# Kernel tuning notes

Measured on AMD Instinct MI355X. Metric: run time of the kernel, lower is better.

The kernel has to match this reference:

```python
import jax, jax.numpy as jnp
import numpy as np

SEM_DIM = 256
AC_DIM = 36
CODEBOOK_SIZE = 8192
FSQ_LEVELS = 21
COMMIT_COST = 0.25
HALF = (FSQ_LEVELS - 1) / 2.0  # 10.0
EPS = 0.001


def setup_inputs() -> dict:
    key = jax.random.key(0)
    k1, k2 = jax.random.split(key)
    z = jax.random.normal(k1, (8, SEM_DIM + AC_DIM, 4096), dtype=jnp.float32)
    lim = 1.0 / CODEBOOK_SIZE
    codebook = jax.random.uniform(k2, (CODEBOOK_SIZE, SEM_DIM), dtype=jnp.float32,
                                  minval=-lim, maxval=lim)
    return {"z": z, "codebook": codebook}


def _round_ste(x):
    return x + jax.lax.stop_gradient(jnp.round(x) - x)


def _vq(z_sem, codebook):
    # z_sem: (B, D, T), codebook: (K, D)
    B, D, T = z_sem.shape
    z_flat = jnp.transpose(z_sem, (0, 2, 1)).reshape(B * T, D)  # (N, D)
    # pairwise squared distances via matmul: ||z||^2 - 2 z.W^T + ||W||^2
    dists = (jnp.sum(z_flat * z_flat, axis=1, keepdims=True)
             - 2.0 * jnp.matmul(z_flat, codebook.T)
             + jnp.sum(codebook * codebook, axis=1)[None, :])  # (N, K)
    indices = jnp.argmin(dists, axis=1)  # (N,)
    z_q_flat = codebook[indices]  # (N, D) gather
    z_q = jnp.transpose(z_q_flat.reshape(B, T, D), (0, 2, 1))  # (B, D, T)
    codebook_loss = jnp.mean((z_q - jax.lax.stop_gradient(z_sem)) ** 2)
    commitment_loss = COMMIT_COST * jnp.mean((jax.lax.stop_gradient(z_q) - z_sem) ** 2)
    loss = codebook_loss + commitment_loss
    z_q_ste = z_sem + jax.lax.stop_gradient(z_q - z_sem)  # straight-through
    return z_q_ste, indices.reshape(B, T), loss


def _fsq(z_ac):
    z_b = jnp.tanh(z_ac) * (HALF + EPS)
    z_q = _round_ste(z_b)
    codes = jnp.clip((z_q + HALF).astype(jnp.int32), 0, FSQ_LEVELS - 1)
    return z_q, codes


def reference(z, codebook):
    z_sem = z[:, :SEM_DIM, :]
    z_ac = z[:, SEM_DIM:, :]
    z_sem_q, sem_indices, vq_loss = _vq(z_sem, codebook)
    z_ac_q, ac_codes = _fsq(z_ac)
    z_q = jnp.concatenate([z_sem_q, z_ac_q], axis=1)
    return (z_q, sem_indices, ac_codes, vq_loss, z_ac_q)
```

## Files before the change

### kernel.cpp

```cpp
#include <hip/hip_runtime.h>
#include <math.h>

#define BB 8
#define DSEM 256
#define DAC 36
#define DTOT 292
#define TT 4096
#define NCB 8192
#define NROWS (BB*TT)

static constexpr size_t O0 = 0;
static constexpr size_t O1 = 9568256;
static constexpr size_t O2 = 9601024;
static constexpr size_t O3 = 10780672;
static constexpr size_t O4 = 10780673;

static constexpr size_t WB_AH   = 0;
static constexpr size_t WB_BH   = 16777216;
static constexpr size_t WB_TMIN = 20971520;
static constexpr size_t WB_CBT  = 37748736;
static constexpr size_t WB_RN   = 46137344;
static constexpr size_t WB_CSQ  = 46268416;
static constexpr size_t WB_LOSS = 46301184;
static constexpr size_t WB_CNT  = 46301192;
static constexpr size_t WB_END  = 46301200;
static constexpr unsigned WL_CAP = 4194304;

typedef _Float16 f16x8 __attribute__((ext_vector_type(8)));
typedef __attribute__((ext_vector_type(4))) float f32x4;

__device__ __forceinline__ void gload_lds16(const void* g, void* lds) {
  __builtin_amdgcn_global_load_lds(
      (const __attribute__((address_space(1))) void*)g,
      (__attribute__((address_space(3))) void*)lds, 16, 0, 0);
}


__global__ __launch_bounds__(256) void k_rn(const float* __restrict__ z,
                                            float* __restrict__ rn) {
  int r = blockIdx.x * 256 + threadIdx.x;
  int b = r >> 12, t = r & 4095;
  const float* p = z + ((size_t)(b * DTOT) << 12) + t;
  double acc = 0.0;
  #pragma unroll 8
  for (int d = 0; d < DSEM; ++d) {
    float v = p[(size_t)d << 12];
    acc += (double)v * (double)v;
  }
  rn[r] = (float)acc;
}

__global__ __launch_bounds__(256) void k_fsq(const float* __restrict__ z,
                                             float* __restrict__ out) {
  int e = blockIdx.x * 256 + threadIdx.x;
  int b = e / (DAC * TT);
  int rem = e - b * (DAC * TT);
  int d = rem >> 12, t = rem & 4095;
  float zv = z[((size_t)(b * DTOT + DSEM + d) << 12) + t];
  float th = (float)tanh((double)zv);
  float zb = th * 10.001f;
  float zq = rintf(zb);
  int code = (int)(zq + 10.0f);
  code = code < 0 ? 0 : (code > 20 ? 20 : code);
  out[O0 + (((size_t)(b * DTOT + DSEM + d)) << 12) + t] = zq;
  out[O2 + e] = (float)code;
  out[O4 + e] = zq;
}


__global__ __launch_bounds__(256) void k_prepB2(const float* __restrict__ cb,
                                                _Float16* __restrict__ Bh,
                                                float* __restrict__ csq,
                                                double* __restrict__ loss,
                                                unsigned* __restrict__ counters) {
  if (blockIdx.x == 0 && threadIdx.x == 0) {
    loss[0] = 0.0; counters[0] = 0u; counters[1] = 0u;
  }
  int e = blockIdx.x * 256 + threadIdx.x;
  float4 v = reinterpret_cast<const float4*>(cb)[e];
  union { _Float16 h[4]; short4 s4; } o;
  o.h[0] = (_Float16)(v.x * -32768.0f);
  o.h[1] = (_Float16)(v.y * -32768.0f);
  o.h[2] = (_Float16)(v.z * -32768.0f);
  o.h[3] = (_Float16)(v.w * -32768.0f);
  reinterpret_cast<short4*>(Bh)[e] = o.s4;
  float s = v.x * v.x + v.y * v.y + v.z * v.z + v.w * v.w;
  for (int off = 32; off; off >>= 1) s += __shfl_xor(s, off);
  if ((threadIdx.x & 63) == 0) csq[e >> 6] = s;
}

__global__ __launch_bounds__(256) void k_prepA(const float* __restrict__ z,
                                               _Float16* __restrict__ Ah,
                                               float* __restrict__ outz) {
  __shared__ float tile[64][65];
  int bid = blockIdx.x;
  int tt = bid & 63, kt = (bid >> 6) & 3, b = bid >> 8;
  int k0 = kt * 64, t0 = tt * 64;
  int tid = threadIdx.x;
  #pragma unroll
  for (int i = 0; i < 16; ++i) {
    int flat = i * 256 + tid;
    int kk = flat >> 6, t2 = flat & 63;
    tile[kk][t2] = z[((size_t)(b * DTOT + k0 + kk) << 12) + t0 + t2];
  }
  __syncthreads();
  float* zTb = outz + (size_t)b * (DTOT * TT);
  #pragma unroll
  for (int i = 0; i < 16; ++i) {
    int flat = i * 256 + tid;
    int t2 = flat >> 6, kk = flat & 63;
    float v = tile[kk][t2];
    Ah[(size_t)(b * 4096 + t0 + t2) * 256 + k0 + kk] = (_Float16)v;
    zTb[(size_t)(t0 + t2) * 256 + k0 + kk] = v;
  }
}

__global__ __launch_bounds__(256) void k_prepC(const float* __restrict__ cb,
                                               float* __restrict__ cbT4) {
  int e = blockIdx.x * 256 + threadIdx.x;
  int c = e & 31, r = e >> 5;
  int u = r >> 6, k4 = r & 63;
  int j = (u << 5) + c;
  float4 v = *reinterpret_cast<const float4*>(cb + (size_t)j * 256 + k4 * 4);
  reinterpret_cast<float4*>(cbT4)[e] = v;
}

__global__ __launch_bounds__(256) void k_gemm(const _Float16* __restrict__ A,
                                              const _Float16* __restrict__ B,
                                              const float* __restrict__ csq,
                                              _Float16* __restrict__ tmin) {
  __shared__ char smraw[128 * 68 * 4];
  _Float16* As = (_Float16*)smraw;
  _Float16* Bs = (_Float16*)(smraw + 16384);
  float* red = (float*)smraw;
  const float SCALE = 6.103515625e-05f;

  int bid = blockIdx.x;
  int wg = (bid & 7) * 2048 + (bid >> 3);
  int mtile = wg >> 6, ntile = wg & 63;
  int rbase = mtile << 7, cbase = ntile << 7;
  int tid = threadIdx.x, lane = tid & 63, wid = tid >> 6;
  int wm = wid >> 1, wn = wid & 1;
  int l15 = lane & 15, l4 = lane >> 4;
  int sw = l15 & 7;

  f32x4 acc[4][4];
  #pragma unroll
  for (int mi = 0; mi < 4; ++mi)
    #pragma unroll
    for (int ni = 0; ni < 4; ++ni) acc[mi][ni] = (f32x4){0.f, 0.f, 0.f, 0.f};

  for (int kt = 0; kt < 4; ++kt) {
    int kb = kt << 6;
    __syncthreads();
    #pragma unroll
    for (int i = 0; i < 4; ++i) {
      int flat = (wid * 4 + i) * 64 + lane;
      int row = flat >> 3;
      int csrc = (flat & 7) ^ (row & 7);
      gload_lds16(A + (size_t)(rbase + row) * 256 + kb + (csrc << 3),
                  (char*)As + flat * 16);
      gload_lds16(B + (size_t)(cbase + row) * 256 + kb + (csrc << 3),
                  (char*)Bs + flat * 16);
    }
    __syncthreads();
    #pragma unroll
    for (int ks = 0; ks < 2; ++ks) {
      int off = ((((ks << 2) + l4) ^ sw) << 3);
      f16x8 af[4], bv[4];
      #pragma unroll
      for (int mi = 0; mi < 4; ++mi)
        af[mi] = *(const f16x8*)(As + ((wm * 64 + mi * 16 + l15) << 6) + off);
      #pragma unroll
      for (int ni = 0; ni < 4; ++ni)
        bv[ni] = *(const f16x8*)(Bs + ((wn * 64 + ni * 16 + l15) << 6) + off);
      #pragma unroll
      for (int mi = 0; mi < 4; ++mi)
        #pragma unroll
        for (int ni = 0; ni < 4; ++ni)
          acc[mi][ni] = __builtin_amdgcn_mfma_f32_16x16x32_f16(af[mi], bv[ni], acc[mi][ni], 0, 0, 0);
    }
  }

  float csv[4];
  #pragma unroll
  for (int ni = 0; ni < 4; ++ni) csv[ni] = csq[cbase + wn * 64 + ni * 16 + l15];

  __syncthreads();
  #pragma unroll
  for (int mi = 0; mi < 4; ++mi) {
    #pragma unroll
    for (int r = 0; r < 4; ++r) {
      int row = wm * 64 + mi * 16 + l4 * 4 + r;
      float v0 = fminf(fmaf(acc[mi][0][r], SCALE, csv[0]),
                       fmaf(acc[mi][1][r], SCALE, csv[1]));
      float v1 = fminf(fmaf(acc[mi][2][r], SCALE, csv[2]),
                       fmaf(acc[mi][3][r], SCALE, csv[3]));
      red[row * 68 + (wn * 2 + 0) * 16 + l15] = v0;
      red[row * 68 + (wn * 2 + 1) * 16 + l15] = v1;
    }
  }
  __syncthreads();
  if (tid < 128) {
    int row = tid;
    const float* rp = red + row * 68;
    union { _Float16 h[4]; short4 s; } uu;
    #pragma unroll
    for (int q = 0; q < 4; ++q) {
      float m = rp[q * 16];
      #pragma unroll
      for (int x = 1; x < 16; ++x) m = fminf(m, rp[q * 16 + x]);
      uu.h[q] = (_Float16)m;
    }
    *reinterpret_cast<short4*>(tmin + (size_t)(rbase + row) * 256 + ntile * 4) = uu.s;
  }
}

__global__ __launch_bounds__(256) void k_cand(const _Float16* __restrict__ tmin,
                                              unsigned* __restrict__ wl,
                                              unsigned* __restrict__ counter,
                                              unsigned long long* __restrict__ result) {
  __shared__ unsigned long long smask[16][4];
  __shared__ unsigned scnt[16];
  __shared__ unsigned soff[16];
  int tid = threadIdx.x;
  int wv = tid >> 6, lane = tid & 63;
  int row0 = blockIdx.x << 4;

  for (int rr = wv; rr < 16; rr += 4) {
    int row = row0 + rr;
    const _Float16* tp = tmin + (size_t)row * 256;
    float v[4];
    #pragma unroll
    for (int i = 0; i < 4; ++i) v[i] = (float)tp[i * 64 + lane];
    float g = fminf(fminf(v[0], v[1]), fminf(v[2], v[3]));
    #pragma unroll
    for (int off = 32; off; off >>= 1) g = fminf(g, __shfl_xor(g, off));
    float thr = g + 2e-4f;
    if (lane == 0) result[row] = 0xFFFFFFFFFFFFFFFFULL;
    unsigned cnt = 0;
    #pragma unroll
    for (int i = 0; i < 4; ++i) {
      unsigned long long mask = __ballot(v[i] <= thr);
      if (lane == 0) smask[rr][i] = mask;
      cnt += (unsigned)__popcll(mask);
    }
    if (lane == 0) scnt[rr] = cnt;
  }
  __syncthreads();
  if (tid == 0) {
    unsigned tot = 0;
    #pragma unroll
    for (int r = 0; r < 16; ++r) { soff[r] = tot; tot += scnt[r]; }
    unsigned base = atomicAdd(counter, tot);
    #pragma unroll
    for (int r = 0; r < 16; ++r) soff[r] += base;
  }
  __syncthreads();
  for (int rr = wv; rr < 16; rr += 4) {
    int row = row0 + rr;
    unsigned off = soff[rr];
    unsigned acc = 0;
    #pragma unroll
    for (int i = 0; i < 4; ++i) {
      unsigned long long mask = smask[rr][i];
      bool c = (mask >> lane) & 1ULL;
      if (c) {
        unsigned rank = acc + (unsigned)__popcll(mask & ((1ULL << lane) - 1ULL));
        unsigned idx = off + rank;
        if (idx < WL_CAP) wl[idx] = ((unsigned)row << 8) | (unsigned)(i * 64 + lane);
      }
      acc += (unsigned)__popcll(mask);
    }
  }
}

__global__ __launch_bounds__(256) void k_scan(const float* __restrict__ zT,
                                              const float* __restrict__ cbT4,
                                              const float* __restrict__ csq,
                                              const float* __restrict__ rn,
                                              const unsigned* __restrict__ wl,
                                              const unsigned* __restrict__ counter,
                                              unsigned long long* __restrict__ result) {
  unsigned total = *counter;
  if (total > WL_CAP) total = WL_CAP;
  int tid = threadIdx.x;
  int gw = blockIdx.x * 4 + (tid >> 6);
  int half = (tid >> 5) & 1, l32 = tid & 31;
  for (unsigned it = (unsigned)(gw * 2 + half); it < total; it += 16384u) {
    unsigned e = wl[it];
    int row = (int)(e >> 8), u = (int)(e & 255u);
    int j = (u << 5) + l32;
    int b = row >> 12, t = row & 4095;
    const float4* zp = reinterpret_cast<const float4*>(
        zT + (size_t)b * (DTOT * TT) + (size_t)t * 256);
    const float4* cp = reinterpret_cast<const float4*>(cbT4) + ((u * 64) * 32 + l32);
    float an = rn[row], cq = csq[j];
    float m0 = 0.f, m1 = 0.f, m2 = 0.f, m3 = 0.f;
    #pragma unroll 8
    for (int k4 = 0; k4 < 64; ++k4) {
      float4 cv = cp[k4 * 32];
      float4 zv = zp[k4];
      m0 = fmaf(zv.x, cv.x, m0);
      m1 = fmaf(zv.y, cv.y, m1);
      m2 = fmaf(zv.z, cv.z, m2);
      m3 = fmaf(zv.w, cv.w, m3);
    }
    float m = (m0 + m1) + (m2 + m3);
    float d = (an - 2.f * m) + cq;
    unsigned long long pk =
        (((unsigned long long)__float_as_uint(d)) << 32) | (unsigned)j;
    #pragma unroll
    for (int off = 16; off; off >>= 1) {
      unsigned long long o = __shfl_xor(pk, off);
      if (o < pk) pk = o;
    }
    if (l32 == 0) atomicMin(result + row, pk);
  }
}

__global__ __launch_bounds__(256) void k_loss(const float* __restrict__ z,
                                              const float* __restrict__ cb,
                                              const unsigned long long* __restrict__ result,
                                              float* __restrict__ out0,
                                              float* __restrict__ out1,
                                              double* __restrict__ loss,
                                              unsigned* __restrict__ done,
                                              float* __restrict__ out3) {
  int e0 = blockIdx.x * 256 + threadIdx.x;
  if (e0 < NROWS) out1[e0] = (float)(unsigned)(result[e0] & 0xFFFFFFFFULL);
  float s = 0.f;
  for (int e = e0; e < BB * DSEM * TT; e += 2048 * 256) {
    int b = e >> 20;
    int rem = e & 1048575;
    int d = rem >> 12, t = rem & 4095;
    int r = (b << 12) + t;
    int j = (int)(unsigned)(result[r] & 0xFFFFFFFFULL);
    float c = cb[(size_t)j * DSEM + d];
    size_t zi = ((size_t)(b * DTOT + d) << 12) + t;
    float zv = z[zi];
    out0[zi] = c;
    float df = c - zv;
    s += df * df;
  }
  for (int off = 32; off; off >>= 1) s += __shfl_xor(s, off);
  __shared__ float ws4[4];
  int lane = threadIdx.x & 63, w = threadIdx.x >> 6;
  if (lane == 0) ws4[w] = s;
  __syncthreads();
  if (threadIdx.x == 0) {
    float tot = ws4[0] + ws4[1] + ws4[2] + ws4[3];
    atomicAdd(loss, (double)tot);
    __threadfence();
    unsigned old = atomicAdd(done, 1u);
    if (old == 2047u) {
      double total = atomicAdd(loss, 0.0);
      out3[0] = (float)(1.25 * total / 8388608.0);
    }
  }
}


__global__ __launch_bounds__(256) void k_csq(const float* __restrict__ cb,
                                             float* __restrict__ csq,
                                             double* __restrict__ loss,
                                             unsigned* __restrict__ counter) {
  if (blockIdx.x == 0 && threadIdx.x == 0) { loss[0] = 0.0; counter[0] = 0u; }
  int w = (blockIdx.x << 2) + (threadIdx.x >> 6);
  int lane = threadIdx.x & 63;
  float4 v = *reinterpret_cast<const float4*>(cb + (size_t)w * DSEM + lane * 4);
  float s = v.x * v.x + v.y * v.y + v.z * v.z + v.w * v.w;
  for (int off = 32; off; off >>= 1) s += __shfl_xor(s, off);
  if (lane == 0) csq[w] = s;
}

__global__ void k_fin(const double* __restrict__ loss, float* __restrict__ out3) {
  out3[0] = (float)(1.25 * loss[0] / 8388608.0);
}

__global__ __launch_bounds__(256) void k_vq(const float* __restrict__ z,
                                            const float* __restrict__ cb,
                                            const float* __restrict__ csq,
                                            const float* __restrict__ rn,
                                            float* __restrict__ pmin,
                                            int* __restrict__ pidx) {
  __shared__ float As[32][132];
  __shared__ float Bs[32][132];
  const int tid = threadIdx.x;
  const int tx = tid & 15, ty = tid >> 4;
  const int mb = blockIdx.x >> 2, s = blockIdx.x & 3;
  const int r0 = mb << 7;
  const int b = r0 >> 12, t0 = r0 & 4095;
  const int nbase = s * 2048;

  int mrow[8], jcol[8];
  #pragma unroll
  for (int i = 0; i < 4; ++i) {
    mrow[i] = ty * 4 + i;  mrow[i + 4] = 64 + ty * 4 + i;
    jcol[i] = tx * 4 + i;  jcol[i + 4] = 64 + tx * 4 + i;
  }
  float an[8];
  #pragma unroll
  for (int i = 0; i < 8; ++i) an[i] = rn[r0 + mrow[i]];

  float rmin[8]; int ridx[8];
  #pragma unroll
  for (int i = 0; i < 8; ++i) { rmin[i] = 3.402823466e38f; ridx[i] = 0; }

  for (int nc = 0; nc < 16; ++nc) {
    const int n0 = nbase + nc * 128;
    float acc[8][8];
    #pragma unroll
    for (int i = 0; i < 8; ++i)
      #pragma unroll
      for (int j = 0; j < 8; ++j) acc[i][j] = 0.f;

    for (int kc = 0; kc < 8; ++kc) {
      const int kb = kc << 5;
      __syncthreads();
      #pragma unroll
      for (int i = 0; i < 4; ++i) {
        int flat = i * 256 + tid;
        int k = flat >> 5, m4 = (flat & 31) << 2;
        float4 vv = *reinterpret_cast<const float4*>(
            z + ((size_t)(b * DTOT + kb + k) << 12) + t0 + m4);
        *reinterpret_cast<float4*>(&As[k][m4]) = vv;
      }
      #pragma unroll
      for (int i = 0; i < 4; ++i) {
        int flat = i * 256 + tid;
        int j = flat >> 3, k4 = (flat & 7) << 2;
        float4 vv = *reinterpret_cast<const float4*>(
            cb + ((size_t)(n0 + j) << 8) + kb + k4);
        Bs[k4 + 0][j] = vv.x; Bs[k4 + 1][j] = vv.y;
        Bs[k4 + 2][j] = vv.z; Bs[k4 + 3][j] = vv.w;
      }
      __syncthreads();
      #pragma unroll 8
      for (int k = 0; k < 32; ++k) {
        float a[8], bv[8];
        *reinterpret_cast<float4*>(&a[0]) = *reinterpret_cast<const float4*>(&As[k][ty * 4]);
        *reinterpret_cast<float4*>(&a[4]) = *reinterpret_cast<const float4*>(&As[k][64 + ty * 4]);
        *reinterpret_cast<float4*>(&bv[0]) = *reinterpret_cast<const float4*>(&Bs[k][tx * 4]);
        *reinterpret_cast<float4*>(&bv[4]) = *reinterpret_cast<const float4*>(&Bs[k][64 + tx * 4]);
        #pragma unroll
        for (int i = 0; i < 8; ++i)
          #pragma unroll
          for (int j = 0; j < 8; ++j) acc[i][j] = fmaf(a[i], bv[j], acc[i][j]);
      }
    }
    float cs[8];
    #pragma unroll
    for (int j = 0; j < 8; ++j) cs[j] = csq[n0 + jcol[j]];
    #pragma unroll
    for (int i = 0; i < 8; ++i) {
      #pragma unroll
      for (int j = 0; j < 8; ++j) {
        float d = (an[i] - 2.f * acc[i][j]) + cs[j];
        int jg = n0 + jcol[j];
        if (d < rmin[i] || (d == rmin[i] && jg < ridx[i])) { rmin[i] = d; ridx[i] = jg; }
      }
    }
  }
  __syncthreads();
  float* redf = &As[0][0];
  int* redi = reinterpret_cast<int*>(&Bs[0][0]);
  #pragma unroll
  for (int i = 0; i < 8; ++i) {
    redf[mrow[i] * 16 + tx] = rmin[i];
    redi[mrow[i] * 16 + tx] = ridx[i];
  }
  __syncthreads();
  if (tid < 128) {
    int row = tid;
    float bestv = redf[row * 16]; int bi = redi[row * 16];
    #pragma unroll
    for (int x = 1; x < 16; ++x) {
      float m = redf[row * 16 + x]; int ii = redi[row * 16 + x];
      if (m < bestv || (m == bestv && ii < bi)) { bestv = m; bi = ii; }
    }
    pmin[(size_t)(r0 + row) * 4 + s] = bestv;
    pidx[(size_t)(r0 + row) * 4 + s] = bi;
  }
}

__global__ __launch_bounds__(256) void k_comb(const float* __restrict__ pmin,
                                              const int* __restrict__ pidx,
                                              int* __restrict__ widx,
                                              float* __restrict__ out1) {
  int r = blockIdx.x * 256 + threadIdx.x;
  float best = pmin[r * 4]; int bi = pidx[r * 4];
  #pragma unroll
  for (int s2 = 1; s2 < 4; ++s2) {
    float m = pmin[r * 4 + s2]; int ii = pidx[r * 4 + s2];
    if (m < best || (m == best && ii < bi)) { best = m; bi = ii; }
  }
  widx[r] = bi;
  out1[r] = (float)bi;
}

__global__ __launch_bounds__(256) void k_loss_fb(const float* __restrict__ z,
                                                 const float* __restrict__ cb,
                                                 const int* __restrict__ idx,
                                                 float* __restrict__ out0,
                                                 double* __restrict__ loss) {
  float s = 0.f;
  for (int e = blockIdx.x * 256 + threadIdx.x; e < BB * DSEM * TT; e += 2048 * 256) {
    int b = e >> 20;
    int rem = e & 1048575;
    int d = rem >> 12, t = rem & 4095;
    int r = (b << 12) + t;
    int j = idx[r];
    float c = cb[(size_t)j * DSEM + d];
    size_t zi = ((size_t)(b * DTOT + d) << 12) + t;
    float zv = z[zi];
    out0[zi] = c;
    float df = c - zv;
    s += df * df;
  }
  for (int off = 32; off; off >>= 1) s += __shfl_xor(s, off);
  __shared__ float ws4[4];
  int lane = threadIdx.x & 63, w = threadIdx.x >> 6;
  if (lane == 0) ws4[w] = s;
  __syncthreads();
  if (threadIdx.x == 0) {
    float tot = ws4[0] + ws4[1] + ws4[2] + ws4[3];
    atomicAdd(loss, (double)tot);
  }
}


extern "C" void kernel_launch(void* const* d_in, const int* in_sizes, int n_in,
                              void* d_out, int out_size, void* d_ws, size_t ws_size,
                              hipStream_t stream) {
  const float* z  = (const float*)d_in[0];
  const float* cb = (const float*)d_in[1];
  float* out = (float*)d_out;

  if (ws_size >= WB_END) {
    char* wsb = (char*)d_ws;
    _Float16* Ah   = (_Float16*)(wsb + WB_AH);
    _Float16* Bh   = (_Float16*)(wsb + WB_BH);
    _Float16* tmin = (_Float16*)(wsb + WB_TMIN);
    float*    cbT4 = (float*)(wsb + WB_CBT);
    float*    rn   = (float*)(wsb + WB_RN);
    float*    csq  = (float*)(wsb + WB_CSQ);
    double*   loss = (double*)(wsb + WB_LOSS);
    unsigned* counters = (unsigned*)(wsb + WB_CNT);
    unsigned* wl = (unsigned*)(wsb + WB_AH);
    unsigned long long* result = (unsigned long long*)(wsb + WB_BH);
    float* zT = out + O0;

    k_prepB2<<<2048, 256, 0, stream>>>(cb, Bh, csq, loss, counters);
    k_rn<<<NROWS / 256, 256, 0, stream>>>(z, rn);
    k_fsq<<<(BB * DAC * TT) / 256, 256, 0, stream>>>(z, out);
    k_prepA<<<2048, 256, 0, stream>>>(z, Ah, zT);
    k_prepC<<<2048, 256, 0, stream>>>(cb, cbT4);
    k_gemm<<<16384, 256, 0, stream>>>(Ah, Bh, csq, tmin);
    k_cand<<<NROWS / 16, 256, 0, stream>>>(tmin, wl, counters, result);
    k_scan<<<2048, 256, 0, stream>>>(zT, cbT4, csq, rn, wl, counters, result);
    k_loss<<<2048, 256, 0, stream>>>(z, cb, result, out + O0, out + O1, loss,
                                     counters + 1, out + O3);
  } else {
    float* wsf = (float*)d_ws;
    float* csq  = wsf;
    float* rn   = wsf + 8192;
    float* pmin = wsf + 40960;
    int*   pidx = (int*)(wsf + 172032);
    int*   widx = (int*)(wsf + 303104);
    double* loss = (double*)(wsf + 335872);
    unsigned* counter = (unsigned*)(wsf + 335876);

    k_csq<<<NCB / 4, 256, 0, stream>>>(cb, csq, loss, counter);
    k_rn<<<NROWS / 256, 256, 0, stream>>>(z, rn);
    k_fsq<<<(BB * DAC * TT) / 256, 256, 0, stream>>>(z, out);
    k_vq<<<(NROWS / 128) * 4, 256, 0, stream>>>(z, cb, csq, rn, pmin, pidx);
    k_comb<<<NROWS / 256, 256, 0, stream>>>(pmin, pidx, widx, out + O1);
    k_loss_fb<<<2048, 256, 0, stream>>>(z, cb, widx, out + O0, loss);
    k_fin<<<1, 1, 0, stream>>>(loss, out + O3);
  }
}
```

Before: 442.5 us.

## Fuse row-norm into prepA, tile output/loss kernel through LDS, widen scan grid

Removes the separate k_rn pass by computing row squared norms inside k_prepA, which now loops over all four k-tiles per block and reduces the double partials in shared memory. The output/loss kernel is restructured to stage a 64-timestep z tile in LDS, gather whole codebook rows with vectorized loads per row, and write the quantized tile back coalesced, replacing the strided per-element gather. k_scan gets a doubled grid with a grid-derived stride. These cut redundant z reads and uncoalesced gathers in exchange for fewer, heavier blocks in prepA and k_out, which may reduce occupancy.

```diff
diff --git a/kernel.cpp b/kernel.cpp
--- a/kernel.cpp
+++ b/kernel.cpp
@@ -35,20 +35,6 @@
       (__attribute__((address_space(3))) void*)lds, 16, 0, 0);
 }
 
-
-__global__ __launch_bounds__(256) void k_rn(const float* __restrict__ z,
-                                            float* __restrict__ rn) {
-  int r = blockIdx.x * 256 + threadIdx.x;
-  int b = r >> 12, t = r & 4095;
-  const float* p = z + ((size_t)(b * DTOT) << 12) + t;
-  double acc = 0.0;
-  #pragma unroll 8
-  for (int d = 0; d < DSEM; ++d) {
-    float v = p[(size_t)d << 12];
-    acc += (double)v * (double)v;
-  }
-  rn[r] = (float)acc;
-}
 
 __global__ __launch_bounds__(256) void k_fsq(const float* __restrict__ z,
                                              float* __restrict__ out) {
@@ -91,27 +77,47 @@
 
 __global__ __launch_bounds__(256) void k_prepA(const float* __restrict__ z,
                                                _Float16* __restrict__ Ah,
-                                               float* __restrict__ outz) {
+                                               float* __restrict__ outz,
+                                               float* __restrict__ rn) {
   __shared__ float tile[64][65];
+  __shared__ double rpart[4][64];
   int bid = blockIdx.x;
-  int tt = bid & 63, kt = (bid >> 6) & 3, b = bid >> 8;
-  int k0 = kt * 64, t0 = tt * 64;
+  int tt = bid & 63, b = bid >> 6;
+  int t0 = tt * 64;
   int tid = threadIdx.x;
-  #pragma unroll
-  for (int i = 0; i < 16; ++i) {
-    int flat = i * 256 + tid;
-    int kk = flat >> 6, t2 = flat & 63;
-    tile[kk][t2] = z[((size_t)(b * DTOT + k0 + kk) << 12) + t0 + t2];
-  }
-  __syncthreads();
+  int t2r = tid & 63, q = tid >> 6;
+  double acc = 0.0;
   float* zTb = outz + (size_t)b * (DTOT * TT);
-  #pragma unroll
-  for (int i = 0; i < 16; ++i) {
-    int flat = i * 256 + tid;
-    int t2 = flat >> 6, kk = flat & 63;
-    float v = tile[kk][t2];
-    Ah[(size_t)(b * 4096 + t0 + t2) * 256 + k0 + kk] = (_Float16)v;
-    zTb[(size_t)(t0 + t2) * 256 + k0 + kk] = v;
+
+  for (int kt = 0; kt < 4; ++kt) {
+    int k0 = kt * 64;
+    #pragma unroll
+    for (int i = 0; i < 16; ++i) {
+      int flat = i * 256 + tid;
+      int kk = flat >> 6, t2 = flat & 63;
+      tile[kk][t2] = z[((size_t)(b * DTOT + k0 + kk) << 12) + t0 + t2];
+    }
+    __syncthreads();
+    #pragma unroll
+    for (int r = 0; r < 16; ++r) {
+      float v = tile[q * 16 + r][t2r];
+      acc += (double)v * (double)v;
+    }
+    #pragma unroll
+    for (int i = 0; i < 16; ++i) {
+      int flat = i * 256 + tid;
+      int t2 = flat >> 6, kk = flat & 63;
+      float v = tile[kk][t2];
+      Ah[(size_t)(b * 4096 + t0 + t2) * 256 + k0 + kk] = (_Float16)v;
+      zTb[(size_t)(t0 + t2) * 256 + k0 + kk] = v;
+    }
+    __syncthreads();
+  }
+  rpart[q][t2r] = acc;
+  __syncthreads();
+  if (tid < 64) {
+    double s = ((rpart[0][tid] + rpart[1][tid]) + (rpart[2][tid] + rpart[3][tid]));
+    rn[(b << 12) + t0 + tid] = (float)s;
   }
 }
 
@@ -285,9 +291,10 @@
   unsigned total = *counter;
   if (total > WL_CAP) total = WL_CAP;
   int tid = threadIdx.x;
+  unsigned stride = gridDim.x * 8u;
   int gw = blockIdx.x * 4 + (tid >> 6);
   int half = (tid >> 5) & 1, l32 = tid & 31;
-  for (unsigned it = (unsigned)(gw * 2 + half); it < total; it += 16384u) {
+  for (unsigned it = (unsigned)(gw * 2 + half); it < total; it += stride) {
     unsigned e = wl[it];
     int row = (int)(e >> 8), u = (int)(e & 255u);
     int j = (u << 5) + l32;
@@ -319,41 +326,76 @@
   }
 }
 
-__global__ __launch_bounds__(256) void k_loss(const float* __restrict__ z,
-                                              const float* __restrict__ cb,
-                                              const unsigned long long* __restrict__ result,
-                                              float* __restrict__ out0,
-                                              float* __restrict__ out1,
-                                              double* __restrict__ loss,
-                                              unsigned* __restrict__ done,
-                                              float* __restrict__ out3) {
-  int e0 = blockIdx.x * 256 + threadIdx.x;
-  if (e0 < NROWS) out1[e0] = (float)(unsigned)(result[e0] & 0xFFFFFFFFULL);
-  float s = 0.f;
-  for (int e = e0; e < BB * DSEM * TT; e += 2048 * 256) {
-    int b = e >> 20;
-    int rem = e & 1048575;
-    int d = rem >> 12, t = rem & 4095;
-    int r = (b << 12) + t;
-    int j = (int)(unsigned)(result[r] & 0xFFFFFFFFULL);
-    float c = cb[(size_t)j * DSEM + d];
-    size_t zi = ((size_t)(b * DTOT + d) << 12) + t;
-    float zv = z[zi];
-    out0[zi] = c;
-    float df = c - zv;
-    s += df * df;
-  }
-  for (int off = 32; off; off >>= 1) s += __shfl_xor(s, off);
-  __shared__ float ws4[4];
-  int lane = threadIdx.x & 63, w = threadIdx.x >> 6;
-  if (lane == 0) ws4[w] = s;
-  __syncthreads();
-  if (threadIdx.x == 0) {
-    float tot = ws4[0] + ws4[1] + ws4[2] + ws4[3];
+__global__ __launch_bounds__(256) void k_out(const float* __restrict__ z,
+                                             const float* __restrict__ cb,
+                                             const unsigned long long* __restrict__ result,
+                                             float* __restrict__ out0,
+                                             float* __restrict__ out1,
+                                             double* __restrict__ loss,
+                                             unsigned* __restrict__ done,
+                                             float* __restrict__ out3) {
+  __shared__ float zs[64][257];
+  __shared__ float hsum[8];
+  int bid = blockIdx.x;
+  int tt = bid & 63, b = bid >> 6;
+  int t0 = tt * 64;
+  int tid = threadIdx.x;
+
+  #pragma unroll 4
+  for (int i = 0; i < 16; ++i) {
+    int d = i * 16 + (tid >> 4);
+    int t4 = (tid & 15) * 4;
+    float4 v = *reinterpret_cast<const float4*>(
+        z + ((size_t)(b * DTOT + d) << 12) + t0 + t4);
+    zs[t4 + 0][d] = v.x; zs[t4 + 1][d] = v.y;
+    zs[t4 + 2][d] = v.z; zs[t4 + 3][d] = v.w;
+  }
+  __syncthreads();
+
+  int hw = tid >> 5, l32 = tid & 31;
+  float lsum = 0.f;
+  for (int p = 0; p < 8; ++p) {
+    int t2 = p * 8 + hw;
+    int row = (b << 12) + t0 + t2;
+    unsigned j = (unsigned)(result[row] & 0xFFFFFFFFULL);
+    if (l32 == 0) out1[row] = (float)j;
+    const float4* cp = reinterpret_cast<const float4*>(cb + (size_t)j * 256);
+    float4 c0 = cp[l32 * 2], c1 = cp[l32 * 2 + 1];
+    int d0 = l32 * 8;
+    float cs = 0.f, df;
+    df = c0.x - zs[t2][d0 + 0]; cs = fmaf(df, df, cs); zs[t2][d0 + 0] = c0.x;
+    df = c0.y - zs[t2][d0 + 1]; cs = fmaf(df, df, cs); zs[t2][d0 + 1] = c0.y;
+    df = c0.z - zs[t2][d0 + 2]; cs = fmaf(df, df, cs); zs[t2][d0 + 2] = c0.z;
+    df = c0.w - zs[t2][d0 + 3]; cs = fmaf(df, df, cs); zs[t2][d0 + 3] = c0.w;
+    df = c1.x - zs[t2][d0 + 4]; cs = fmaf(df, df, cs); zs[t2][d0 + 4] = c1.x;
+    df = c1.y - zs[t2][d0 + 5]; cs = fmaf(df, df, cs); zs[t2][d0 + 5] = c1.y;
+    df = c1.z - zs[t2][d0 + 6]; cs = fmaf(df, df, cs); zs[t2][d0 + 6] = c1.z;
+    df = c1.w - zs[t2][d0 + 7]; cs = fmaf(df, df, cs); zs[t2][d0 + 7] = c1.w;
+    lsum += cs;
+  }
+  #pragma unroll
+  for (int off = 16; off; off >>= 1) lsum += __shfl_xor(lsum, off);
+  if (l32 == 0) hsum[hw] = lsum;
+  __syncthreads();
+
+  #pragma unroll 4
+  for (int i = 0; i < 16; ++i) {
+    int d = i * 16 + (tid >> 4);
+    int t4 = (tid & 15) * 4;
+    float4 v;
+    v.x = zs[t4 + 0][d]; v.y = zs[t4 + 1][d];
+    v.z = zs[t4 + 2][d]; v.w = zs[t4 + 3][d];
+    *reinterpret_cast<float4*>(
+        out0 + ((size_t)(b * DTOT + d) << 12) + t0 + t4) = v;
+  }
+
+  if (tid == 0) {
+    float tot = ((hsum[0] + hsum[1]) + (hsum[2] + hsum[3])) +
+                ((hsum[4] + hsum[5]) + (hsum[6] + hsum[7]));
     atomicAdd(loss, (double)tot);
     __threadfence();
     unsigned old = atomicAdd(done, 1u);
-    if (old == 2047u) {
+    if (old == 511u) {
       double total = atomicAdd(loss, 0.0);
       out3[0] = (float)(1.25 * total / 8388608.0);
     }
@@ -372,6 +414,20 @@
   float s = v.x * v.x + v.y * v.y + v.z * v.z + v.w * v.w;
   for (int off = 32; off; off >>= 1) s += __shfl_xor(s, off);
   if (lane == 0) csq[w] = s;
+}
+
+__global__ __launch_bounds__(256) void k_rn(const float* __restrict__ z,
+                                            float* __restrict__ rn) {
+  int r = blockIdx.x * 256 + threadIdx.x;
+  int b = r >> 12, t = r & 4095;
+  const float* p = z + ((size_t)(b * DTOT) << 12) + t;
+  double acc = 0.0;
+  #pragma unroll 8
+  for (int d = 0; d < DSEM; ++d) {
+    float v = p[(size_t)d << 12];
+    acc += (double)v * (double)v;
+  }
+  rn[r] = (float)acc;
 }
 
 __global__ void k_fin(const double* __restrict__ loss, float* __restrict__ out3) {
@@ -552,15 +608,14 @@
     float* zT = out + O0;
 
     k_prepB2<<<2048, 256, 0, stream>>>(cb, Bh, csq, loss, counters);
-    k_rn<<<NROWS / 256, 256, 0, stream>>>(z, rn);
     k_fsq<<<(BB * DAC * TT) / 256, 256, 0, stream>>>(z, out);
-    k_prepA<<<2048, 256, 0, stream>>>(z, Ah, zT);
+    k_prepA<<<512, 256, 0, stream>>>(z, Ah, zT, rn);
     k_prepC<<<2048, 256, 0, stream>>>(cb, cbT4);
     k_gemm<<<16384, 256, 0, stream>>>(Ah, Bh, csq, tmin);
     k_cand<<<NROWS / 16, 256, 0, stream>>>(tmin, wl, counters, result);
-    k_scan<<<2048, 256, 0, stream>>>(zT, cbT4, csq, rn, wl, counters, result);
-    k_loss<<<2048, 256, 0, stream>>>(z, cb, result, out + O0, out + O1, loss,
-                                     counters + 1, out + O3);
+    k_scan<<<4096, 256, 0, stream>>>(zT, cbT4, csq, rn, wl, counters, result);
+    k_out<<<512, 256, 0, stream>>>(z, cb, result, out + O0, out + O1, loss,
+                                   counters + 1, out + O3);
   } else {
     float* wsf = (float*)d_ws;
     float* csq  = wsf;
```

After: 372.1 us. 15.9% less time.
